# Kernel optimization log

Measured on AMD Instinct MI355X. Metric: run time of the kernel, lower is better.

Reference implementation:

```python
import jax, jax.numpy as jnp
import numpy as np

B, E, H, V, D2, T = 128, 512, 512, 32000, 1024, 17

def setup_inputs() -> dict:
    key = jax.random.key(0)
    ks = jax.random.split(key, 13)
    s = 0.02
    return {
        "features": jax.random.normal(ks[0], (B, 512), dtype=jnp.float32),
        "captions": jax.random.randint(ks[1], (B, T), 0, V, dtype=jnp.int32),
        "W_enc": jax.random.normal(ks[2], (512, E), dtype=jnp.float32) * s,
        "b_enc": jnp.zeros((E,), dtype=jnp.float32),
        "emb": jax.random.normal(ks[3], (V, E), dtype=jnp.float32) * s,
        "W_ih": jax.random.normal(ks[4], (4 * H, E), dtype=jnp.float32) * s,
        "b_ih": jnp.zeros((4 * H,), dtype=jnp.float32),
        "W_hh": jax.random.normal(ks[5], (4 * H, H), dtype=jnp.float32) * s,
        "b_hh": jnp.zeros((4 * H,), dtype=jnp.float32),
        "W_d2": jax.random.normal(ks[6], (H, D2), dtype=jnp.float32) * s,
        "b_d2": jnp.zeros((D2,), dtype=jnp.float32),
        "W_last": jax.random.normal(ks[7], (D2, V), dtype=jnp.float32) * s,
        "b_last": jnp.zeros((V,), dtype=jnp.float32),
    }


def reference(features, captions, W_enc, b_enc, emb, W_ih, b_ih, W_hh, b_hh, W_d2, b_d2, W_last, b_last):
    # encoder_last: project frozen-resnet features [B,512] -> [B,E]
    feat = features @ W_enc + b_enc
    # embed captions[:, :-1] -> [B,16,E], prepend image feature -> [B,17,E]
    e = emb[captions[:, :-1]]
    x = jnp.concatenate([feat[:, None, :], e], axis=1)  # [B,T,E]

    def step(carry, xt):
        h, c = carry
        gates = xt @ W_ih.T + b_ih + h @ W_hh.T + b_hh  # [B,4H]
        i, f, g, o = jnp.split(gates, 4, axis=-1)  # PyTorch LSTMCell gate order
        i, f, o = jax.nn.sigmoid(i), jax.nn.sigmoid(f), jax.nn.sigmoid(o)
        g = jnp.tanh(g)
        c = f * c + i * g
        h = o * jnp.tanh(c)
        return (h, c), h

    h0 = jnp.zeros((x.shape[0], H), dtype=x.dtype)
    c0 = jnp.zeros((x.shape[0], H), dtype=x.dtype)
    _, hs = jax.lax.scan(step, (h0, c0), jnp.swapaxes(x, 0, 1))  # [T,B,H]
    hs = jnp.swapaxes(hs, 0, 1)  # [B,T,H]

    out = jax.nn.relu(hs @ W_d2 + b_d2)       # [B,T,D2]
    logits = out @ W_last + b_last            # [B,T,V]
    return jax.nn.softmax(logits, axis=2)
```

## Files before the change

kernel.cpp:

```cpp
#include <hip/hip_runtime.h>
#include <hip/hip_bf16.h>

#define B_   128
#define T_   17
#define E_   512
#define H_   512
#define V_   32000
#define D2_  1024
#define MR_  (B_*T_)

typedef __attribute__((ext_vector_type(8))) short short8;
typedef __attribute__((ext_vector_type(4))) float f32x4;

__device__ __forceinline__ unsigned short f2b(float f) {
  unsigned u = __float_as_uint(f);
  u += 0x7FFFu + ((u >> 16) & 1u);
  return (unsigned short)(u >> 16);
}
__device__ __forceinline__ float sigf(float x) { return 1.f / (1.f + __expf(-x)); }
__device__ __forceinline__ float tanhfast(float x) {
  x = fminf(fmaxf(x, -15.f), 15.f);
  float e = __expf(2.f * x);
  return (e - 1.f) / (e + 1.f);
}

__device__ __forceinline__ void async16(const void* g, void* l) {
  __builtin_amdgcn_global_load_lds((const __attribute__((address_space(1))) unsigned int*)g,
                                   (__attribute__((address_space(3))) unsigned int*)l,
                                   16, 0, 0);
}

template<int EPI, int SWZ>
__global__ __launch_bounds__(256, 2)
void gemm_bt(const unsigned short* __restrict__ A,
             const unsigned short* __restrict__ Bt,
             void* __restrict__ C,
             const float* __restrict__ bias0,
             const float* __restrict__ bias1,
             int N, int K, int nbm, int nwork)
{
  __shared__ unsigned short sA[128 * 32];
  __shared__ unsigned short sB[128 * 32];

  int f = blockIdx.x;
  if constexpr (SWZ) {
    int per = (nwork + 7) >> 3;
    f = (f & 7) * per + (f >> 3);
    if (f >= nwork) return;
  }
  const size_t bm = (size_t)(f % nbm) * 128;
  const size_t bn = (size_t)(f / nbm) * 128;

  const int tid  = threadIdx.x;
  const int lane = tid & 63;
  const int wave = tid >> 6;
  const int wm   = wave & 1;
  const int wn   = wave >> 1;

  const int sRow   = wave * 32 + (lane >> 2);
  const int gchunk = (lane & 3) ^ ((sRow >> 2) & 3);

  const unsigned short* gA  = A  + (bm + sRow)      * (size_t)K + gchunk * 8;
  const unsigned short* gA2 = A  + (bm + sRow + 16) * (size_t)K + gchunk * 8;
  const unsigned short* gB  = Bt + (bn + sRow)      * (size_t)K + gchunk * 8;
  const unsigned short* gB2 = Bt + (bn + sRow + 16) * (size_t)K + gchunk * 8;

  unsigned short* lA  = &sA[wave * 1024];
  unsigned short* lA2 = &sA[wave * 1024 + 512];
  unsigned short* lB  = &sB[wave * 1024];
  unsigned short* lB2 = &sB[wave * 1024 + 512];

  f32x4 acc[4][4] = {};
  const int fm = lane & 15;
  const int q  = lane >> 4;

  for (int kt = 0; kt < K; kt += 32) {
    async16(gA  + kt, lA);
    async16(gA2 + kt, lA2);
    async16(gB  + kt, lB);
    async16(gB2 + kt, lB2);
    __syncthreads();

    short8 af[4], bfv[4];
#pragma unroll
    for (int i = 0; i < 4; i++) {
      int ra = wm * 64 + i * 16 + fm;
      af[i]  = *(const short8*)&sA[ra * 32 + ((q ^ ((ra >> 2) & 3)) * 8)];
      int rb = wn * 64 + i * 16 + fm;
      bfv[i] = *(const short8*)&sB[rb * 32 + ((q ^ ((rb >> 2) & 3)) * 8)];
    }
#pragma unroll
    for (int i = 0; i < 4; i++)
#pragma unroll
      for (int j = 0; j < 4; j++)
        acc[i][j] = __builtin_amdgcn_mfma_f32_16x16x32_bf16(af[i], bfv[j], acc[i][j], 0, 0, 0);
    __syncthreads();
  }

#pragma unroll
  for (int i = 0; i < 4; i++) {
#pragma unroll
    for (int j = 0; j < 4; j++) {
      size_t col = bn + wn * 64 + j * 16 + fm;
      float bv = 0.f;
      if constexpr (EPI == 0) {
        size_t oc = ((col & 3) << 9) + (col >> 2);
        bv = bias0[oc] + bias1[oc];
      }
      if constexpr (EPI == 2 || EPI == 3 || EPI == 4) bv = bias0[col];
#pragma unroll
      for (int r = 0; r < 4; r++) {
        size_t row = bm + wm * 64 + i * 16 + q * 4 + r;
        float v = acc[i][j][r] + bv;
        if constexpr (EPI == 2) {
          v = v > 0.f ? v : 0.f;
          ((unsigned short*)C)[row * N + col] = f2b(v);
        } else if constexpr (EPI == 3) {
          ((unsigned short*)C)[row * N + col] = f2b(v);
        } else {
          ((float*)C)[row * N + col] = v;
        }
      }
    }
  }
}

__global__ __launch_bounds__(256)
void lstm_step(const unsigned short* __restrict__ hprev,
               const unsigned short* __restrict__ Whh,
               const float* __restrict__ Gt,
               float* __restrict__ c,
               unsigned short* __restrict__ hout,
               unsigned short* __restrict__ hsb,
               int t)
{
  __shared__ char smem[131072];
  unsigned short* sA = (unsigned short*)smem;
  unsigned short* sB = (unsigned short*)(smem + 65536);
  float* gl = (float*)smem;

  const int tid  = threadIdx.x;
  const int lane = tid & 63;
  const int wave = tid >> 6;
  const int wm   = wave & 1;
  const int wn   = wave >> 1;
  const int n0   = blockIdx.x * 128;

  const int lr = lane >> 5;
  const int lp = lane & 31;

  f32x4 acc[4][4] = {};
  const int fm = lane & 15;
  const int q  = lane >> 4;

  for (int kt = 0; kt < 512; kt += 256) {
#pragma unroll
    for (int s = 0; s < 16; s++) {
      int row = wave * 32 + s * 2 + lr;
      int gch = lp ^ (row & 7);
      async16(hprev + (size_t)row * 512 + kt + gch * 8,
              sA + wave * 8192 + s * 512 + lane * 8);
      async16(Whh + (size_t)(n0 + row) * 512 + kt + gch * 8,
              sB + wave * 8192 + s * 512 + lane * 8);
    }
    __syncthreads();

#pragma unroll
    for (int kk = 0; kk < 8; kk++) {
      int ch = kk * 4 + q;
      short8 af[4], bfv[4];
#pragma unroll
      for (int i = 0; i < 4; i++) {
        int ra = wm * 64 + i * 16 + fm;
        af[i]  = *(const short8*)&sA[ra * 256 + ((ch ^ (ra & 7)) * 8)];
        int rb = wn * 64 + i * 16 + fm;
        bfv[i] = *(const short8*)&sB[rb * 256 + ((ch ^ (rb & 7)) * 8)];
      }
#pragma unroll
      for (int i = 0; i < 4; i++)
#pragma unroll
        for (int j = 0; j < 4; j++)
          acc[i][j] = __builtin_amdgcn_mfma_f32_16x16x32_bf16(af[i], bfv[j], acc[i][j], 0, 0, 0);
    }
    __syncthreads();
  }

#pragma unroll
  for (int i = 0; i < 4; i++)
#pragma unroll
    for (int j = 0; j < 4; j++)
#pragma unroll
      for (int r = 0; r < 4; r++)
        gl[(wm * 64 + i * 16 + q * 4 + r) * 132 + wn * 64 + j * 16 + fm] = acc[i][j][r];
  __syncthreads();

#pragma unroll
  for (int it = 0; it < 16; it++) {
    int p   = it * 256 + tid;
    int row = p >> 5;
    int ul  = p & 31;
    float4 a4 = *(float4*)&gl[row * 132 + ul * 4];
    float4 G4 = *(const float4*)&Gt[row * 2048 + n0 + ul * 4];
    float gi = a4.x + G4.x, gf = a4.y + G4.y, gg = a4.z + G4.z, go = a4.w + G4.w;
    int gu  = (n0 >> 2) + ul;
    int idx = row * 512 + gu;
    float cn = sigf(gf) * c[idx] + sigf(gi) * tanhfast(gg);
    c[idx] = cn;
    float hn = sigf(go) * tanhfast(cn);
    unsigned short h16 = f2b(hn);
    hout[idx] = h16;
    hsb[((size_t)row * T_ + t) * 512 + gu] = h16;
  }
}

__global__ void lstm_point0(const float* __restrict__ G0, float* __restrict__ c,
                            unsigned short* __restrict__ hb, unsigned short* __restrict__ hsb) {
  int idx = blockIdx.x * 256 + threadIdx.x;
  int b = idx >> 9, u = idx & 511;
  float4 g4 = ((const float4*)(G0 + (size_t)b * 2048))[u];
  float cn = sigf(g4.x) * tanhfast(g4.z);
  c[idx] = cn;
  float hn = sigf(g4.w) * tanhfast(cn);
  unsigned short h16 = f2b(hn);
  hb[idx] = h16;
  hsb[((size_t)b * T_ + 0) * 512 + u] = h16;
}

__global__ void permute_cvt2(const float* __restrict__ Wih, const float* __restrict__ Whh,
                             unsigned short* __restrict__ dih, unsigned short* __restrict__ dhh) {
  int p = blockIdx.x;
  const float* src = (p < 2048) ? Wih : Whh;
  unsigned short* dst = (p < 2048) ? dih : dhh;
  int pp = p & 2047;
  int ir = ((pp & 3) << 9) + (pp >> 2);
  float4 v = ((const float4*)(src + (size_t)ir * 512))[threadIdx.x];
  ushort4 o;
  o.x = f2b(v.x); o.y = f2b(v.y); o.z = f2b(v.z); o.w = f2b(v.w);
  ((ushort4*)(dst + (size_t)p * 512))[threadIdx.x] = o;
}

__global__ void transpose_cvt(const float* __restrict__ src, unsigned short* __restrict__ dst,
                              int K, int N) {
  __shared__ float tile[32][33];
  int n0 = blockIdx.x * 32, k0 = blockIdx.y * 32;
  int tcol = threadIdx.x & 31, trow = threadIdx.x >> 5;
  for (int r = trow; r < 32; r += 8)
    tile[r][tcol] = src[(size_t)(k0 + r) * N + n0 + tcol];
  __syncthreads();
  for (int r = trow; r < 32; r += 8)
    dst[(size_t)(n0 + r) * K + k0 + tcol] = f2b(tile[tcol][r]);
}

__global__ __launch_bounds__(256) void encode(const float* __restrict__ features,
                                              const float* __restrict__ W_enc,
                                              const float* __restrict__ b_enc,
                                              unsigned short* __restrict__ xb) {
  __shared__ float fs[512];
  int b = blockIdx.y, e = blockIdx.x * 256 + threadIdx.x;
  fs[threadIdx.x]       = features[b * 512 + threadIdx.x];
  fs[threadIdx.x + 256] = features[b * 512 + threadIdx.x + 256];
  __syncthreads();
  float acc = 0.f;
#pragma unroll 8
  for (int k = 0; k < 512; k++) acc += fs[k] * W_enc[(size_t)k * 512 + e];
  xb[(size_t)b * 512 + e] = f2b(acc + b_enc[e]);
}

__global__ void embed_k(const int* __restrict__ captions, const float* __restrict__ emb,
                        unsigned short* __restrict__ xb) {
  int t = blockIdx.x + 1, b = blockIdx.y;
  int tok = captions[b * T_ + (t - 1)];
  float4 v = ((const float4*)(emb + (size_t)tok * 512))[threadIdx.x];
  ushort4 o;
  o.x = f2b(v.x); o.y = f2b(v.y); o.z = f2b(v.z); o.w = f2b(v.w);
  ((ushort4*)(xb + (size_t)(t * B_ + b) * 512))[threadIdx.x] = o;
}

__global__ __launch_bounds__(1024) void softmax_b(const unsigned short* __restrict__ lg,
                                                  float* __restrict__ out) {
  __shared__ float ps[1024];
  const uint4* r4 = (const uint4*)(lg + (size_t)blockIdx.x * V_);
  float* orow = out + (size_t)blockIdx.x * V_;
  int tid = threadIdx.x;
  float v[4][8];
  float s = 0.f;
#pragma unroll
  for (int u = 0; u < 4; u++) {
    int i = u * 1024 + tid;
    if (i < 4000) {
      uint4 w = r4[i];
      unsigned a[4] = {w.x, w.y, w.z, w.w};
#pragma unroll
      for (int k = 0; k < 4; k++) {
        float lo = __uint_as_float(a[k] << 16);
        float hi = __uint_as_float(a[k] & 0xffff0000u);
        float e0 = __expf(lo), e1 = __expf(hi);
        v[u][2 * k] = e0; v[u][2 * k + 1] = e1;
        s += e0 + e1;
      }
    }
  }
  ps[tid] = s;
  __syncthreads();
  for (int o = 512; o > 0; o >>= 1) {
    if (tid < o) ps[tid] += ps[tid + o];
    __syncthreads();
  }
  float inv = 1.f / ps[0];
#pragma unroll
  for (int u = 0; u < 4; u++) {
    int i = u * 1024 + tid;
    if (i < 4000) {
      float4 o1 = {v[u][0] * inv, v[u][1] * inv, v[u][2] * inv, v[u][3] * inv};
      float4 o2 = {v[u][4] * inv, v[u][5] * inv, v[u][6] * inv, v[u][7] * inv};
      ((float4*)(orow + (size_t)i * 8))[0] = o1;
      ((float4*)(orow + (size_t)i * 8))[1] = o2;
    }
  }
}

__global__ __launch_bounds__(1024) void softmax_f(float* __restrict__ out) {
  __shared__ float ps[1024];
  float* r = out + (size_t)blockIdx.x * V_;
  int tid = threadIdx.x;
  float v[32];
  float s = 0.f;
#pragma unroll
  for (int u = 0; u < 32; u++) {
    int i = u * 1024 + tid;
    if (i < V_) { float e = __expf(r[i]); v[u] = e; s += e; }
  }
  ps[tid] = s;
  __syncthreads();
  for (int o = 512; o > 0; o >>= 1) {
    if (tid < o) ps[tid] += ps[tid + o];
    __syncthreads();
  }
  float inv = 1.f / ps[0];
#pragma unroll
  for (int u = 0; u < 32; u++) {
    int i = u * 1024 + tid;
    if (i < V_) r[i] = v[u] * inv;
  }
}

extern "C" void kernel_launch(void* const* d_in, const int* in_sizes, int n_in,
                              void* d_out, int out_size, void* d_ws, size_t ws_size,
                              hipStream_t stream) {
  const float* features = (const float*)d_in[0];
  const int*   captions = (const int*)d_in[1];
  const float* W_enc  = (const float*)d_in[2];
  const float* b_enc  = (const float*)d_in[3];
  const float* emb    = (const float*)d_in[4];
  const float* W_ih   = (const float*)d_in[5];
  const float* b_ih   = (const float*)d_in[6];
  const float* W_hh   = (const float*)d_in[7];
  const float* b_hh   = (const float*)d_in[8];
  const float* W_d2   = (const float*)d_in[9];
  const float* b_d2   = (const float*)d_in[10];
  const float* W_last = (const float*)d_in[11];
  const float* b_last = (const float*)d_in[12];
  float* out = (float*)d_out;

  char* ws = (char*)d_ws;
  size_t off = 0;
  auto alloc = [&](size_t bytes) -> void* {
    void* p = ws + off;
    off += (bytes + 255) & ~(size_t)255;
    return p;
  };
  unsigned short* xb     = (unsigned short*)alloc((size_t)MR_ * E_ * 2);
  unsigned short* Wb_ih  = (unsigned short*)alloc((size_t)4 * H_ * E_ * 2);
  unsigned short* Wb_hh  = (unsigned short*)alloc((size_t)4 * H_ * H_ * 2);
  unsigned short* Wb_d2t = (unsigned short*)alloc((size_t)D2_ * H_ * 2);
  unsigned short* Wb_lt  = (unsigned short*)alloc((size_t)V_ * D2_ * 2);
  float*          G      = (float*)alloc((size_t)MR_ * 4 * H_ * 4);
  float*          cst    = (float*)alloc((size_t)B_ * H_ * 4);
  unsigned short* hb0    = (unsigned short*)alloc((size_t)B_ * H_ * 2);
  unsigned short* hb1    = (unsigned short*)alloc((size_t)B_ * H_ * 2);
  unsigned short* hsb    = (unsigned short*)alloc((size_t)MR_ * H_ * 2);
  unsigned short* outb   = (unsigned short*)alloc((size_t)MR_ * D2_ * 2);
  unsigned short* lgb    = (unsigned short*)alloc((size_t)MR_ * V_ * 2);
  const bool bf16_logits = (off <= ws_size);
  (void)in_sizes; (void)n_in; (void)out_size;

  permute_cvt2<<<4096, 128, 0, stream>>>(W_ih, W_hh, Wb_ih, Wb_hh);
  transpose_cvt<<<dim3(D2_ / 32, H_ / 32), 256, 0, stream>>>(W_d2, Wb_d2t, H_, D2_);

  encode<<<dim3(2, B_), 256, 0, stream>>>(features, W_enc, b_enc, xb);
  embed_k<<<dim3(T_ - 1, B_), 128, 0, stream>>>(captions, emb, xb);

  gemm_bt<0, 0><<<17 * 16, 256, 0, stream>>>(xb, Wb_ih, G, b_ih, b_hh, 4 * H_, E_, 17, 17 * 16);

  lstm_point0<<<B_ * H_ / 256, 256, 0, stream>>>(G, cst, hb0, hsb);
  for (int t = 1; t < T_; t++) {
    unsigned short* hp = (t & 1) ? hb0 : hb1;
    unsigned short* hc = (t & 1) ? hb1 : hb0;
    lstm_step<<<16, 256, 0, stream>>>(hp, Wb_hh, G + (size_t)t * B_ * 4 * H_, cst, hc, hsb, t);
  }

  transpose_cvt<<<dim3(V_ / 32, D2_ / 32), 256, 0, stream>>>(W_last, Wb_lt, D2_, V_);

  gemm_bt<2, 0><<<17 * 8, 256, 0, stream>>>(hsb, Wb_d2t, outb, b_d2, nullptr, D2_, H_, 17, 17 * 8);

  const int nwork = 17 * (V_ / 128);
  const int per   = (nwork + 7) / 8;
  if (bf16_logits) {
    gemm_bt<3, 1><<<8 * per, 256, 0, stream>>>(outb, Wb_lt, lgb, b_last, nullptr, V_, D2_, 17, nwork);
    softmax_b<<<MR_, 1024, 0, stream>>>(lgb, out);
  } else {
    gemm_bt<4, 1><<<8 * per, 256, 0, stream>>>(outb, Wb_lt, out, b_last, nullptr, V_, D2_, 17, nwork);
    softmax_f<<<MR_, 1024, 0, stream>>>(out);
  }
}
```

Measured before the change: 949.3 us.

## Add 256x256-tile pipelined MFMA GEMM for vocabulary projection

Adds a new 512-thread GEMM kernel that uses 256x256 output tiles, double-buffered async global-to-LDS staging with XOR swizzling, and interleaved barriers and priority hints around the MFMA blocks. The large logits GEMM (2176x32000x1024) now uses this kernel in place of the 128-wide tile kernel. The goal is more data reuse per tile and better overlap of loads with MFMA work. The last M tile is clamped to overlap the previous one, so some rows are computed twice, and the large LDS footprint and register use may limit occupancy.

```diff
diff --git a/kernel.cpp b/kernel.cpp
--- a/kernel.cpp
+++ b/kernel.cpp
@@ -124,6 +124,145 @@
     }
   }
 }
+
+#define STG(gp, lb, row0, kt) do { \
+    async16((gp) + (size_t)(row0) * K + (kt),       (lb) + (row0) * 64); \
+    async16((gp) + (size_t)((row0) + 8) * K + (kt), (lb) + ((row0) + 8) * 64); \
+  } while (0)
+
+template<int EPI>
+__global__ __launch_bounds__(512, 2)
+void gemm256(const unsigned short* __restrict__ A,
+             const unsigned short* __restrict__ Bt,
+             void* __restrict__ C,
+             const float* __restrict__ bias0,
+             int N, int K, int M, int nbm, int nwork)
+{
+  __shared__ unsigned short sA[2][256 * 64];
+  __shared__ unsigned short sB[2][256 * 64];
+
+  int f = blockIdx.x;
+  const int per = (nwork + 7) >> 3;
+  f = (f & 7) * per + (f >> 3);
+  if (f >= nwork) return;
+  int bmx = (f % nbm) * 256;
+  if (bmx > M - 256) bmx = M - 256;
+  const size_t bm = (size_t)bmx;
+  const size_t bn = (size_t)(f / nbm) * 256;
+
+  const int tid  = threadIdx.x;
+  const int lane = tid & 63;
+  const int wave = tid >> 6;
+  const int wm   = wave >> 2;
+  const int wn   = wave & 3;
+  const int fm   = lane & 15;
+  const int q    = lane >> 4;
+
+  const int cs = (((lane & 7) ^ (lane >> 3)) << 3);
+  const unsigned short* gA = A  + (bm + (lane >> 3)) * (size_t)K + cs;
+  const unsigned short* gB = Bt + (bn + (lane >> 3)) * (size_t)K + cs;
+
+  const int NT = K >> 6;
+  const int arow0 = (wave & 3) * 16 + (wave >> 2) * 128;
+  const int arow1 = arow0 + 64;
+  const int brow0 = wave * 16;
+  const int brow1 = brow0 + 128;
+
+  STG(gB, sB[0], brow0, 0);
+  STG(gB, sB[0], brow1, 0);
+  STG(gA, sA[0], arow0, 0);
+  STG(gA, sA[0], arow1, 0);
+  if (NT > 1) {
+    STG(gB, sB[1], brow0, 64);
+    STG(gB, sB[1], brow1, 64);
+    STG(gA, sA[1], arow0, 64);
+    asm volatile("s_waitcnt vmcnt(6)" ::: "memory");
+  } else {
+    asm volatile("s_waitcnt vmcnt(0)" ::: "memory");
+  }
+  __builtin_amdgcn_s_barrier();
+
+  f32x4 acc[8][4] = {};
+  short8 breg[4][2];
+
+  for (int t = 0; t < NT; ++t) {
+    const int bi = t & 1;
+    const unsigned short* sa = sA[bi];
+    const unsigned short* sb = sB[bi];
+    const int kt1 = (t + 1) << 6;
+    const int kt2 = (t + 2) << 6;
+    const bool st1 = (t + 1) < NT;
+    const bool st2 = (t + 2) < NT;
+
+#pragma unroll
+    for (int mq = 0; mq < 4; ++mq) {
+      short8 a[2][2];
+#pragma unroll
+      for (int ff = 0; ff < 2; ff++) {
+        const int r = wm * 128 + (2 * mq + ff) * 16 + fm;
+#pragma unroll
+        for (int ks = 0; ks < 2; ks++)
+          a[ff][ks] = *(const short8*)&sa[r * 64 + (((ks * 4 + q) ^ (r & 7)) << 3)];
+      }
+      if (mq == 0) {
+#pragma unroll
+        for (int j = 0; j < 4; j++) {
+          const int r = wn * 64 + j * 16 + fm;
+#pragma unroll
+          for (int ks = 0; ks < 2; ks++)
+            breg[j][ks] = *(const short8*)&sb[r * 64 + (((ks * 4 + q) ^ (r & 7)) << 3)];
+        }
+        if (st1) STG(gA, sA[bi ^ 1], arow1, kt1);
+      } else if (mq == 1) {
+        if (st2) STG(gB, sB[bi], brow0, kt2);
+      } else if (mq == 2) {
+        if (st2) STG(gB, sB[bi], brow1, kt2);
+      } else {
+        if (st2) STG(gA, sA[bi], arow0, kt2);
+      }
+
+      asm volatile("" ::: "memory");
+      __builtin_amdgcn_s_barrier();
+      asm volatile("s_waitcnt lgkmcnt(0)" ::: "memory");
+      __builtin_amdgcn_sched_barrier(0);
+      __builtin_amdgcn_s_setprio(1);
+#pragma unroll
+      for (int ff = 0; ff < 2; ff++)
+#pragma unroll
+        for (int j = 0; j < 4; j++)
+#pragma unroll
+          for (int ks = 0; ks < 2; ks++)
+            acc[2 * mq + ff][j] =
+              __builtin_amdgcn_mfma_f32_16x16x32_bf16(a[ff][ks], breg[j][ks],
+                                                      acc[2 * mq + ff][j], 0, 0, 0);
+      __builtin_amdgcn_s_setprio(0);
+      __builtin_amdgcn_sched_barrier(0);
+      if (mq == 3) {
+        if (st2)      asm volatile("s_waitcnt vmcnt(6)" ::: "memory");
+        else if (st1) asm volatile("s_waitcnt vmcnt(0)" ::: "memory");
+      }
+      asm volatile("" ::: "memory");
+      __builtin_amdgcn_s_barrier();
+    }
+  }
+
+#pragma unroll
+  for (int i = 0; i < 8; i++) {
+#pragma unroll
+    for (int j = 0; j < 4; j++) {
+      const size_t col = bn + wn * 64 + j * 16 + fm;
+      const float bv = bias0[col];
+#pragma unroll
+      for (int r = 0; r < 4; r++) {
+        const size_t row = bm + wm * 128 + i * 16 + q * 4 + r;
+        const float v = acc[i][j][r] + bv;
+        if constexpr (EPI == 3) ((unsigned short*)C)[row * (size_t)N + col] = f2b(v);
+        else                    ((float*)C)[row * (size_t)N + col] = v;
+      }
+    }
+  }
+}
+#undef STG
 
 __global__ __launch_bounds__(256)
 void lstm_step(const unsigned short* __restrict__ hprev,
@@ -403,13 +542,14 @@
 
   gemm_bt<2, 0><<<17 * 8, 256, 0, stream>>>(hsb, Wb_d2t, outb, b_d2, nullptr, D2_, H_, 17, 17 * 8);
 
-  const int nwork = 17 * (V_ / 128);
-  const int per   = (nwork + 7) / 8;
+  const int nbm2   = 9;
+  const int nwork2 = nbm2 * (V_ / 256);
+  const int per2   = (nwork2 + 7) / 8;
   if (bf16_logits) {
-    gemm_bt<3, 1><<<8 * per, 256, 0, stream>>>(outb, Wb_lt, lgb, b_last, nullptr, V_, D2_, 17, nwork);
+    gemm256<3><<<8 * per2, 512, 0, stream>>>(outb, Wb_lt, lgb, b_last, V_, D2_, MR_, nbm2, nwork2);
     softmax_b<<<MR_, 1024, 0, stream>>>(lgb, out);
   } else {
-    gemm_bt<4, 1><<<8 * per, 256, 0, stream>>>(outb, Wb_lt, out, b_last, nullptr, V_, D2_, 17, nwork);
+    gemm256<4><<<8 * per2, 512, 0, stream>>>(outb, Wb_lt, out, b_last, V_, D2_, MR_, nbm2, nwork2);
     softmax_f<<<MR_, 1024, 0, stream>>>(out);
   }
 }
```

Result: no change. 943.6 us (-0.6%).
